# Optimization experiments

Measured on AMD Instinct MI355X. Metric: run time of the kernel, lower is better.

The kernel has to match this reference:

```python
import jax, jax.numpy as jnp
import numpy as np


def setup_inputs() -> dict:
    key = jax.random.key(0)
    k1, k2 = jax.random.split(key)
    B, H, W, C = 16, 4, 900, 256
    input_1 = jax.random.normal(k1, (B, H, W, C), dtype=jnp.float32)
    input_2 = jax.random.normal(k2, (B, H, W, C), dtype=jnp.float32)
    return {"input_1": input_1, "input_2": input_2}


def reference(input_1, input_2):
    # Original op: circularly pad input_1 along W (shift by n_pad), frame into W
    # overlapping windows of length W, multiply by input_2 and sum over (H, W, C).
    # Equivalent math: out[b, s] = sum_w <x1[b, :, (s + w + n_pad) % W, :],
    #                                     x2[b, :, w, :]>  (inner product over H, C).
    # We compute the [B, W, W] Gram matrix with a GEMM, then reduce the circular
    # diagonal bands -- avoids materializing the W-times framed [B, H, W, W, C].
    B, H, W, C = input_1.shape
    n_pad = W // 2
    D = H * C
    a1 = jnp.transpose(input_1, (0, 2, 1, 3)).reshape(B, W, D)  # [B, W, H*C]
    a2 = jnp.transpose(input_2, (0, 2, 1, 3)).reshape(B, W, D)
    gram = jnp.einsum('bid,bjd->bij', a1, a2)  # gram[b, i, j] = <x1_i, x2_j>
    s = jnp.arange(W)[:, None]   # shift index
    w = jnp.arange(W)[None, :]   # window position
    idx = (s + w + n_pad) % W    # [W, W] circular gather indices
    out = jnp.sum(gram[:, idx, w], axis=-1)  # [B, W]
    return out
```

## Files before the change

kernel.cpp:

```cpp
#include <hip/hip_runtime.h>
#include <stdint.h>

typedef __attribute__((ext_vector_type(8))) short short8;
typedef __attribute__((ext_vector_type(8))) unsigned short ushort8;
typedef __attribute__((ext_vector_type(4))) float floatx4;

#define W_DIM 900
#define NPAD  450
#define TM    256
#define TN    128
#define SLAB_E   32768
#define BATCH_E  1048576

__device__ __forceinline__ unsigned short f2bf(float f) {
  unsigned int u = __builtin_bit_cast(unsigned int, f);
  return (unsigned short)((u + 0x8000u) >> 16);
}

__device__ __forceinline__ void async16(const void* g, void* l) {
  __builtin_amdgcn_global_load_lds(
      (const __attribute__((address_space(1))) void*)g,
      (__attribute__((address_space(3))) void*)l, 16, 0, 0);
}

__global__ void convert_kernel(const float* __restrict__ X1,
                               const float* __restrict__ X2,
                               unsigned short* __restrict__ dA,
                               unsigned short* __restrict__ dB) {
  const int wt = blockIdx.x;
  const int h  = blockIdx.y;
  const int bz = blockIdx.z;
  const int b  = bz & 15;
  const float* __restrict__ src = (bz >> 4) ? X2 : X1;
  unsigned short* __restrict__ dst = (bz >> 4) ? dB : dA;

  __shared__ __align__(16) unsigned short T[64 * 264];

  const int t  = threadIdx.x;
  const int c8 = (t & 31) << 3;
#pragma unroll
  for (int i = 0; i < 8; ++i) {
    const int wl = i * 8 + (t >> 5);
    const int wg = wt * 64 + wl;
    ushort8 o = (ushort8)0;
    if (wg < W_DIM) {
      const float* p = src + (((size_t)(b * 4 + h) * W_DIM + wg) << 8) + c8;
      float4 v0 = *(const float4*)p;
      float4 v1 = *(const float4*)(p + 4);
      o[0] = f2bf(v0.x); o[1] = f2bf(v0.y); o[2] = f2bf(v0.z); o[3] = f2bf(v0.w);
      o[4] = f2bf(v1.x); o[5] = f2bf(v1.y); o[6] = f2bf(v1.z); o[7] = f2bf(v1.w);
    }
    *(ushort8*)&T[wl * 264 + c8] = o;
  }
  __syncthreads();

  const int wl = t >> 2;
  const int wg = wt * 64 + wl;
  const int ch = t & 3;
  const int c0 = ch ^ (wl & 3);
#pragma unroll
  for (int s = 0; s < 8; ++s) {
    ushort8 v = *(const ushort8*)&T[wl * 264 + s * 32 + c0 * 8];
    const size_t off =
        ((size_t)b * BATCH_E) + (size_t)(h * 8 + s) * SLAB_E + (size_t)wg * 32 + ch * 8;
    *(ushort8*)&dst[off] = v;
  }
}

__global__ __launch_bounds__(256, 2)
void gemm_band_kernel(const unsigned short* __restrict__ A,
                      const unsigned short* __restrict__ B,
                      float* __restrict__ out) {
  const int x    = blockIdx.x;
  const int b    = x & 15;
  const int pair = x >> 4;
  const int it   = pair >> 3;
  const int jt   = pair & 7;

  __shared__ __align__(16) unsigned char smem[49152];
  unsigned short* As = (unsigned short*)smem;
  unsigned short* Bs = As + 16384;

  const int tid  = threadIdx.x;
  const int lane = tid & 63;
  const int warp = tid >> 6;
  const int wm   = warp >> 1;
  const int wn   = warp & 1;

  const unsigned short* gAlane =
      A + (size_t)b * BATCH_E + (size_t)(it * TM + warp * 64) * 32 + lane * 8;
  const unsigned short* gBlane =
      B + (size_t)b * BATCH_E + (size_t)(jt * TN + warp * 32) * 32 + lane * 8;
  unsigned short* lA = As + warp * 64 * 32 + lane * 8;
  unsigned short* lB = Bs + warp * 32 * 32 + lane * 8;

  floatx4 acc[8][4];
#pragma unroll
  for (int i = 0; i < 8; ++i)
#pragma unroll
    for (int j = 0; j < 4; ++j) acc[i][j] = (floatx4)0.0f;

  const int quad = lane >> 4;
  const int r16  = lane & 15;
  const int csw  = (quad ^ (r16 & 3)) * 8;
  const unsigned short* ArowBase = As + (wm * 128 + r16) * 32 + csw;
  const unsigned short* BrowBase = Bs + (wn * 64 + r16) * 32 + csw;

  for (int kt = 0; kt < 16; ++kt) {
    __syncthreads();
    const size_t ko = (size_t)kt * (2 * SLAB_E);
#pragma unroll
    for (int s = 0; s < 2; ++s) {
#pragma unroll
      for (int g = 0; g < 4; ++g)
        async16(gAlane + ko + s * SLAB_E + g * 512, lA + s * 8192 + g * 512);
#pragma unroll
      for (int g = 0; g < 2; ++g)
        async16(gBlane + ko + s * SLAB_E + g * 512, lB + s * 4096 + g * 512);
    }
    __syncthreads();

#pragma unroll
    for (int s = 0; s < 2; ++s) {
      short8 af[8], bf[4];
#pragma unroll
      for (int mi = 0; mi < 8; ++mi)
        af[mi] = *(const short8*)(ArowBase + s * 8192 + mi * 512);
#pragma unroll
      for (int ni = 0; ni < 4; ++ni)
        bf[ni] = *(const short8*)(BrowBase + s * 4096 + ni * 512);
#pragma unroll
      for (int mi = 0; mi < 8; ++mi)
#pragma unroll
        for (int ni = 0; ni < 4; ++ni)
          acc[mi][ni] = __builtin_amdgcn_mfma_f32_16x16x32_bf16(
              af[mi], bf[ni], acc[mi][ni], 0, 0, 0);
    }
  }

  __syncthreads();
  float* Ep = (float*)smem;
  const int dbase = it * TM - jt * TN - NPAD;

  for (int p = 0; p < 4; ++p) {
    if (wm == (p >> 1)) {
      const int mib = (p & 1) * 4;
#pragma unroll
      for (int mo = 0; mo < 4; ++mo)
#pragma unroll
        for (int ni = 0; ni < 4; ++ni)
#pragma unroll
          for (int rr = 0; rr < 4; ++rr) {
            const int lr = mo * 16 + quad * 4 + rr;
            const int c  = wn * 64 + ni * 16 + r16;
            Ep[lr * 132 + c] = acc[mib + mo][ni][rr];
          }
    }
    __syncthreads();
    if (tid < 191) {
      const int d = tid - 127;
      int k0 = d > 0 ? d : 0;
      int k1 = 128 + d; if (k1 > 64) k1 = 64;
      float s = 0.0f;
      for (int k = k0; k < k1; ++k) s += Ep[k * 132 + (k - d)];
      int dg = dbase + p * 64 + d;
      int sidx = dg % W_DIM;
      if (sidx < 0) sidx += W_DIM;
      atomicAdd(&out[b * W_DIM + sidx], s);
    }
    __syncthreads();
  }
}

__global__ void naive_kernel(const float* __restrict__ x1,
                             const float* __restrict__ x2,
                             float* __restrict__ out) {
  const int s = blockIdx.x;
  const int b = blockIdx.y;
  const int c = threadIdx.x;
  float acc = 0.0f;
  for (int h = 0; h < 4; ++h) {
    const float* p1 = x1 + (size_t)(b * 4 + h) * W_DIM * 256;
    const float* p2 = x2 + (size_t)(b * 4 + h) * W_DIM * 256;
    for (int w = 0; w < W_DIM; ++w) {
      int w1 = s + w + NPAD;
      if (w1 >= W_DIM) w1 -= W_DIM;
      if (w1 >= W_DIM) w1 -= W_DIM;
      acc += p1[(size_t)w1 * 256 + c] * p2[(size_t)w * 256 + c];
    }
  }
  for (int off = 32; off > 0; off >>= 1) acc += __shfl_down(acc, off, 64);
  __shared__ float red[4];
  if ((threadIdx.x & 63) == 0) red[threadIdx.x >> 6] = acc;
  __syncthreads();
  if (threadIdx.x == 0)
    out[b * W_DIM + s] = red[0] + red[1] + red[2] + red[3];
}

extern "C" void kernel_launch(void* const* d_in, const int* in_sizes, int n_in,
                              void* d_out, int out_size, void* d_ws, size_t ws_size,
                              hipStream_t stream) {
  const float* x1 = (const float*)d_in[0];
  const float* x2 = (const float*)d_in[1];
  float* out = (float*)d_out;

  hipMemsetAsync(d_out, 0, (size_t)out_size * sizeof(float), stream);

  const size_t need = (size_t)2 * 16 * BATCH_E * sizeof(unsigned short);
  if (ws_size >= need) {
    unsigned short* dA = (unsigned short*)d_ws;
    unsigned short* dB = dA + (size_t)16 * BATCH_E;
    convert_kernel<<<dim3(16, 4, 32), 256, 0, stream>>>(x1, x2, dA, dB);
    gemm_band_kernel<<<dim3(512), 256, 0, stream>>>(dA, dB, out);
  } else {
    naive_kernel<<<dim3(W_DIM, 16), 256, 0, stream>>>(x1, x2, out);
  }
}
```

Baseline: 187.1 us.

## Double-buffer GEMM LDS tiles and batch global loads in convert kernel

The GEMM main loop changes from a load-then-compute loop over k-steps of two slabs to a 32-step loop over single slabs. Two LDS buffers alternate, so the async global-to-LDS load of the next slab is issued before the MFMAs on the current slab, and there is one barrier per step. The convert kernel now issues all sixteen float4 loads before any bf16 conversion and LDS store, to raise memory-level parallelism. The cost is more registers in the convert kernel. The GEMM also relies on a single barrier per step to cover both the async-load visibility and buffer reuse.

```diff
diff --git a/kernel.cpp b/kernel.cpp
--- a/kernel.cpp
+++ b/kernel.cpp
@@ -36,21 +36,30 @@
 
   __shared__ __align__(16) unsigned short T[64 * 264];
 
-  const int t  = threadIdx.x;
-  const int c8 = (t & 31) << 3;
+  const int t   = threadIdx.x;
+  const int c8  = (t & 31) << 3;
+  const int wl0 = t >> 5;
+
+  const float4 fz = make_float4(0.f, 0.f, 0.f, 0.f);
+  float4 v[16];
 #pragma unroll
   for (int i = 0; i < 8; ++i) {
-    const int wl = i * 8 + (t >> 5);
-    const int wg = wt * 64 + wl;
-    ushort8 o = (ushort8)0;
+    const int wg = wt * 64 + i * 8 + wl0;
+    v[2 * i] = fz; v[2 * i + 1] = fz;
     if (wg < W_DIM) {
       const float* p = src + (((size_t)(b * 4 + h) * W_DIM + wg) << 8) + c8;
-      float4 v0 = *(const float4*)p;
-      float4 v1 = *(const float4*)(p + 4);
-      o[0] = f2bf(v0.x); o[1] = f2bf(v0.y); o[2] = f2bf(v0.z); o[3] = f2bf(v0.w);
-      o[4] = f2bf(v1.x); o[5] = f2bf(v1.y); o[6] = f2bf(v1.z); o[7] = f2bf(v1.w);
-    }
-    *(ushort8*)&T[wl * 264 + c8] = o;
+      v[2 * i]     = *(const float4*)p;
+      v[2 * i + 1] = *(const float4*)(p + 4);
+    }
+  }
+#pragma unroll
+  for (int i = 0; i < 8; ++i) {
+    ushort8 o;
+    o[0] = f2bf(v[2*i].x);   o[1] = f2bf(v[2*i].y);
+    o[2] = f2bf(v[2*i].z);   o[3] = f2bf(v[2*i].w);
+    o[4] = f2bf(v[2*i+1].x); o[5] = f2bf(v[2*i+1].y);
+    o[6] = f2bf(v[2*i+1].z); o[7] = f2bf(v[2*i+1].w);
+    *(ushort8*)&T[(i * 8 + wl0) * 264 + c8] = o;
   }
   __syncthreads();
 
@@ -60,10 +69,10 @@
   const int c0 = ch ^ (wl & 3);
 #pragma unroll
   for (int s = 0; s < 8; ++s) {
-    ushort8 v = *(const ushort8*)&T[wl * 264 + s * 32 + c0 * 8];
+    ushort8 vv = *(const ushort8*)&T[wl * 264 + s * 32 + c0 * 8];
     const size_t off =
         ((size_t)b * BATCH_E) + (size_t)(h * 8 + s) * SLAB_E + (size_t)wg * 32 + ch * 8;
-    *(ushort8*)&dst[off] = v;
+    *(ushort8*)&dst[off] = vv;
   }
 }
 
@@ -78,8 +87,7 @@
   const int jt   = pair & 7;
 
   __shared__ __align__(16) unsigned char smem[49152];
-  unsigned short* As = (unsigned short*)smem;
-  unsigned short* Bs = As + 16384;
+  unsigned short* SB = (unsigned short*)smem;
 
   const int tid  = threadIdx.x;
   const int lane = tid & 63;
@@ -87,12 +95,12 @@
   const int wm   = warp >> 1;
   const int wn   = warp & 1;
 
-  const unsigned short* gAlane =
+  const unsigned short* gA =
       A + (size_t)b * BATCH_E + (size_t)(it * TM + warp * 64) * 32 + lane * 8;
-  const unsigned short* gBlane =
+  const unsigned short* gB =
       B + (size_t)b * BATCH_E + (size_t)(jt * TN + warp * 32) * 32 + lane * 8;
-  unsigned short* lA = As + warp * 64 * 32 + lane * 8;
-  unsigned short* lB = Bs + warp * 32 * 32 + lane * 8;
+  const int lAoff = warp * 2048 + lane * 8;
+  const int lBoff = 8192 + warp * 1024 + lane * 8;
 
   floatx4 acc[8][4];
 #pragma unroll
@@ -103,42 +111,45 @@
   const int quad = lane >> 4;
   const int r16  = lane & 15;
   const int csw  = (quad ^ (r16 & 3)) * 8;
-  const unsigned short* ArowBase = As + (wm * 128 + r16) * 32 + csw;
-  const unsigned short* BrowBase = Bs + (wn * 64 + r16) * 32 + csw;
-
-  for (int kt = 0; kt < 16; ++kt) {
+  const int aBase = (wm * 128 + r16) * 32 + csw;
+  const int bBase = 8192 + (wn * 64 + r16) * 32 + csw;
+
+#pragma unroll
+  for (int g = 0; g < 4; ++g) async16(gA + g * 512, SB + lAoff + g * 512);
+#pragma unroll
+  for (int g = 0; g < 2; ++g) async16(gB + g * 512, SB + lBoff + g * 512);
+  __syncthreads();
+
+  for (int kt = 0; kt < 32; ++kt) {
+    const int cur = (kt & 1) * 12288;
+    const int nxt = 12288 - cur;
+    if (kt < 31) {
+      const size_t ko = (size_t)(kt + 1) * SLAB_E;
+#pragma unroll
+      for (int g = 0; g < 4; ++g)
+        async16(gA + ko + g * 512, SB + nxt + lAoff + g * 512);
+#pragma unroll
+      for (int g = 0; g < 2; ++g)
+        async16(gB + ko + g * 512, SB + nxt + lBoff + g * 512);
+    }
+
+    short8 af[8], bf[4];
+#pragma unroll
+    for (int mi = 0; mi < 8; ++mi)
+      af[mi] = *(const short8*)(SB + cur + aBase + mi * 512);
+#pragma unroll
+    for (int ni = 0; ni < 4; ++ni)
+      bf[ni] = *(const short8*)(SB + cur + bBase + ni * 512);
+#pragma unroll
+    for (int mi = 0; mi < 8; ++mi)
+#pragma unroll
+      for (int ni = 0; ni < 4; ++ni)
+        acc[mi][ni] = __builtin_amdgcn_mfma_f32_16x16x32_bf16(
+            af[mi], bf[ni], acc[mi][ni], 0, 0, 0);
+
     __syncthreads();
-    const size_t ko = (size_t)kt * (2 * SLAB_E);
-#pragma unroll
-    for (int s = 0; s < 2; ++s) {
-#pragma unroll
-      for (int g = 0; g < 4; ++g)
-        async16(gAlane + ko + s * SLAB_E + g * 512, lA + s * 8192 + g * 512);
-#pragma unroll
-      for (int g = 0; g < 2; ++g)
-        async16(gBlane + ko + s * SLAB_E + g * 512, lB + s * 4096 + g * 512);
-    }
-    __syncthreads();
-
-#pragma unroll
-    for (int s = 0; s < 2; ++s) {
-      short8 af[8], bf[4];
-#pragma unroll
-      for (int mi = 0; mi < 8; ++mi)
-        af[mi] = *(const short8*)(ArowBase + s * 8192 + mi * 512);
-#pragma unroll
-      for (int ni = 0; ni < 4; ++ni)
-        bf[ni] = *(const short8*)(BrowBase + s * 4096 + ni * 512);
-#pragma unroll
-      for (int mi = 0; mi < 8; ++mi)
-#pragma unroll
-        for (int ni = 0; ni < 4; ++ni)
-          acc[mi][ni] = __builtin_amdgcn_mfma_f32_16x16x32_bf16(
-              af[mi], bf[ni], acc[mi][ni], 0, 0, 0);
-    }
-  }
-
-  __syncthreads();
+  }
+
   float* Ep = (float*)smem;
   const int dbase = it * TM - jt * TN - NPAD;
 
```

After: 188.9 us. No clear change (+1.0%).
